# Performance work log

Measured on AMD Instinct MI355X. Metric: run time of the kernel, lower is better.

## Reference

```python
import jax, jax.numpy as jnp
import numpy as np

H = 256
G = H // 4
RBF = 16
CUTOFF = 10.0
N_ATOMS = 500000
N_BLOCKS = 50000


def _layernorm(x, g, b, eps=1e-5):
    m = jnp.mean(x, axis=-1, keepdims=True)
    v = jnp.var(x, axis=-1, keepdims=True)
    return (x - m) / jnp.sqrt(v + eps) * g + b


def setup_inputs() -> dict:
    key = jax.random.key(0)
    ks = jax.random.split(key, 16)
    def rn(k, shp, scale=0.02):
        return jax.random.normal(k, shp, dtype=jnp.float32) * scale
    return {
        "atom_features": jax.random.normal(ks[0], (N_ATOMS, H), dtype=jnp.float32),
        "atom_positions": jax.random.normal(ks[1], (N_ATOMS, 3), dtype=jnp.float32),
        "block_features": jax.random.normal(ks[2], (N_BLOCKS, H), dtype=jnp.float32),
        "block_id": jnp.sort(jax.random.randint(ks[3], (N_ATOMS,), 0, N_BLOCKS)),
        "rbf_centers": jnp.linspace(0.0, CUTOFF, RBF).astype(jnp.float32),
        "rbf_widths": jnp.full((RBF,), CUTOFF / RBF, dtype=jnp.float32),
        "Wg": rn(ks[4], (RBF, G)), "bg": jnp.zeros((G,), jnp.float32),
        "Wq": rn(ks[5], (H, H)), "bq": jnp.zeros((H,), jnp.float32),
        "Wk": rn(ks[6], (H + G, H)), "bk": jnp.zeros((H,), jnp.float32),
        "Wv": rn(ks[7], (H + G, H)), "bv": jnp.zeros((H,), jnp.float32),
        "Wc1": rn(ks[8], (H, H)), "bc1": jnp.zeros((H,), jnp.float32),
        "Wc2": rn(ks[9], (H, H)), "bc2": jnp.zeros((H,), jnp.float32),
        "Wf1": rn(ks[10], (H, 2 * H)), "bf1": jnp.zeros((2 * H,), jnp.float32),
        "Wf2": rn(ks[11], (2 * H, H)), "bf2": jnp.zeros((H,), jnp.float32),
        "ln1_g": jnp.ones((H,), jnp.float32), "ln1_b": jnp.zeros((H,), jnp.float32),
        "ln2_g": jnp.ones((H,), jnp.float32), "ln2_b": jnp.zeros((H,), jnp.float32),
    }


def reference(atom_features, atom_positions, block_features, block_id,
              rbf_centers, rbf_widths, Wg, bg, Wq, bq, Wk, bk, Wv, bv,
              Wc1, bc1, Wc2, bc2, Wf1, bf1, Wf2, bf2,
              ln1_g, ln1_b, ln2_g, ln2_b):
    nb = block_features.shape[0]
    seg = block_id
    # per-block geometry: centroid, relative distance, RBF expansion
    ones = jnp.ones((atom_features.shape[0],), atom_features.dtype)
    counts = jax.ops.segment_sum(ones, seg, num_segments=nb)
    centroids = jax.ops.segment_sum(atom_positions, seg, num_segments=nb) / jnp.maximum(counts, 1.0)[:, None]
    rel = atom_positions - centroids[seg]                      # [N, 3]
    d = jnp.linalg.norm(rel, axis=1)                           # [N]
    rbf = jnp.exp(-(d[:, None] - rbf_centers[None, :]) ** 2 / (2.0 * rbf_widths[None, :] ** 2))  # [N, RBF]
    geom = rbf @ Wg + bg                                       # [N, G]
    aug = jnp.concatenate([atom_features, geom], axis=1)       # [N, H+G]
    # cross-attention: one query per block, keys/values are block atoms
    Q = block_features @ Wq + bq                               # [NB, H]
    K = aug @ Wk + bk                                          # [N, H]
    V = aug @ Wv + bv                                          # [N, H]
    scale = 1.0 / np.sqrt(float(H))
    scores = jnp.sum(Q[seg] * K, axis=1) * scale               # [N]
    m = jax.ops.segment_max(scores, seg, num_segments=nb)
    m = jnp.where(jnp.isfinite(m), m, 0.0)
    e = jnp.exp(scores - m[seg])
    denom = jnp.maximum(jax.ops.segment_sum(e, seg, num_segments=nb), 1e-20)
    w = e / denom[seg]                                         # segment softmax weights
    context = jax.ops.segment_sum(w[:, None] * V, seg, num_segments=nb)  # [NB, H]
    upd = jax.nn.relu(context @ Wc1 + bc1) @ Wc2 + bc2         # context MLP (dropout=identity, eval)
    h = _layernorm(atom_features + upd[seg], ln1_g, ln1_b)     # scatter update back to atoms
    ffn = jax.nn.relu(h @ Wf1 + bf1) @ Wf2 + bf2
    return _layernorm(h + ffn, ln2_g, ln2_b)
```

## Files before the change

### kernel.cpp

```cpp
#include <hip/hip_runtime.h>
#include <hip/hip_bf16.h>


typedef __hip_bfloat16 bf16;
typedef __attribute__((ext_vector_type(8))) short bf16x8;
typedef __attribute__((ext_vector_type(4))) float f32x4;

__device__ __forceinline__ float b2f(bf16 v) { return __bfloat162float(v); }
__device__ __forceinline__ float us2f(unsigned short u) {
  union { unsigned int v; float f; } c; c.v = ((unsigned int)u) << 16; return c.f;
}
__device__ __forceinline__ unsigned short f2bu(float x) {
  bf16 t = __float2bfloat16(x);
  unsigned short u; __builtin_memcpy(&u, &t, 2); return u;
}
__device__ __forceinline__ float4 ld4(const float* p) {
  return *reinterpret_cast<const float4*>(p);
}
__device__ __forceinline__ float4 ldnt4(const float* p) {
  f32x4 v = __builtin_nontemporal_load(reinterpret_cast<const f32x4*>(p));
  return make_float4(v.x, v.y, v.z, v.w);
}
__device__ __forceinline__ float wsum(float v) {
#pragma unroll
  for (int o = 32; o > 0; o >>= 1) v += __shfl_xor(v, o, 64);
  return v;
}
__device__ __forceinline__ bf16x8 lds_frag(const unsigned short* base, int stride,
                                           int row, int k) {
  return *reinterpret_cast<const bf16x8*>(base + row * stride +
                                          (k ^ ((row & 7) << 3)));
}

__global__ void bounds_k(const int* __restrict__ seg, int* __restrict__ bs,
                         int* __restrict__ be, int N) {
  int i = blockIdx.x * 256 + threadIdx.x;
  if (i >= N) return;
  int b = seg[i];
  if (i == 0 || seg[i - 1] != b) bs[b] = i;
  if (i == N - 1 || seg[i + 1] != b) be[b] = i + 1;
}

__global__ void cent_k(const float* __restrict__ pos, const int* __restrict__ bs,
                       const int* __restrict__ be, float* __restrict__ cent, int NB) {
  int b = blockIdx.x * 256 + threadIdx.x;
  if (b >= NB) return;
  int s0 = bs[b], s1 = be[b];
  float sx = 0.f, sy = 0.f, sz = 0.f;
  for (int i = s0; i < s1; ++i) {
    sx += pos[(size_t)i * 3 + 0];
    sy += pos[(size_t)i * 3 + 1];
    sz += pos[(size_t)i * 3 + 2];
  }
  float inv = 1.f / fmaxf((float)(s1 - s0), 1.f);
  cent[(size_t)b * 3 + 0] = sx * inv;
  cent[(size_t)b * 3 + 1] = sy * inv;
  cent[(size_t)b * 3 + 2] = sz * inv;
}

__global__ __launch_bounds__(256) void geom_k(
    const float* __restrict__ pos, const int* __restrict__ seg,
    const float* __restrict__ cent, const float* __restrict__ centers,
    const float* __restrict__ widths, const float* __restrict__ Wg,
    const float* __restrict__ bg, bf16* __restrict__ geom, int N) {
  __shared__ float sWg[16][64];
  __shared__ float sc[16], sw[16], sbg[64];
  int t = threadIdx.x;
  if (t < 16) {
    sc[t] = centers[t];
    float w = widths[t];
    sw[t] = 1.f / (2.f * w * w);
  }
  for (int j = t; j < 1024; j += 256) sWg[j >> 6][j & 63] = Wg[j];
  if (t < 64) sbg[t] = bg[t];
  __syncthreads();
  int i = blockIdx.x * 256 + t;
  if (i >= N) return;
  int b = seg[i];
  float dx = pos[(size_t)i * 3 + 0] - cent[(size_t)b * 3 + 0];
  float dy = pos[(size_t)i * 3 + 1] - cent[(size_t)b * 3 + 1];
  float dz = pos[(size_t)i * 3 + 2] - cent[(size_t)b * 3 + 2];
  float d = sqrtf(dx * dx + dy * dy + dz * dz);
  float r[16];
#pragma unroll
  for (int j = 0; j < 16; ++j) {
    float dd = d - sc[j];
    r[j] = expf(-dd * dd * sw[j]);
  }
  bf16* gp = geom + (size_t)i * 64;
  for (int g0 = 0; g0 < 64; g0 += 4) {
    float a0 = sbg[g0], a1 = sbg[g0 + 1], a2 = sbg[g0 + 2], a3 = sbg[g0 + 3];
#pragma unroll
    for (int j = 0; j < 16; ++j) {
      float rj = r[j];
      a0 += rj * sWg[j][g0];
      a1 += rj * sWg[j][g0 + 1];
      a2 += rj * sWg[j][g0 + 2];
      a3 += rj * sWg[j][g0 + 3];
    }
    ushort4 o;
    o.x = f2bu(a0); o.y = f2bu(a1); o.z = f2bu(a2); o.w = f2bu(a3);
    *reinterpret_cast<ushort4*>(gp + g0) = o;
  }
}

__global__ void tr_k(const float* __restrict__ in, unsigned short* __restrict__ out,
                     int K, int N) {
  int idx = blockIdx.x * 256 + threadIdx.x;
  if (idx >= N * K) return;
  int n = idx / K, k = idx % K;
  out[idx] = f2bu(in[(size_t)k * N + n]);
}
__global__ void cast_k(const float* __restrict__ in, unsigned short* __restrict__ out,
                       int n) {
  int idx = blockIdx.x * 256 + threadIdx.x;
  if (idx < n) out[idx] = f2bu(in[idx]);
}

__global__ void pack1_k(const float* __restrict__ Wf1,
                        unsigned short* __restrict__ P) {
  int idx = blockIdx.x * 256 + threadIdx.x;
  if (idx >= 512 * 256) return;
  int e = idx & 7;
  int l = (idx >> 3) & 63;
  int blk = idx >> 9;
  int ks = blk & 7, wv = (blk >> 3) & 7, q = blk >> 6;
  int n = q * 128 + wv * 16 + (l & 15);
  int k = ks * 32 + (l >> 4) * 8 + e;
  P[idx] = f2bu(Wf1[(size_t)k * 512 + n]);
}
__global__ void pack2_k(const float* __restrict__ Wf2,
                        unsigned short* __restrict__ P) {
  int idx = blockIdx.x * 256 + threadIdx.x;
  if (idx >= 512 * 256) return;
  int e = idx & 7;
  int l = (idx >> 3) & 63;
  int blk = idx >> 9;
  int ks = blk & 3, q = (blk >> 2) & 3, nt = (blk >> 4) & 1, wv = blk >> 5;
  int n = wv * 32 + nt * 16 + (l & 15);
  int k = q * 128 + ks * 32 + (l >> 4) * 8 + e;
  P[idx] = f2bu(Wf2[(size_t)k * 256 + n]);
}

__global__ __launch_bounds__(512, 4) void blk1_k(
    const float* __restrict__ bfeat, const unsigned short* __restrict__ WqT,
    const float* __restrict__ bq, const unsigned short* __restrict__ WkC,
    const float* __restrict__ bk, float* __restrict__ u, float* __restrict__ cb,
    int NB) {
  __shared__ unsigned short x_lds[64 * 256];
  __shared__ unsigned short q_lds[64 * 256];
  const int t = threadIdx.x;
  const int lane = t & 63, wv = t >> 6, l15 = lane & 15, lhi = lane >> 4;
  const int r0 = blockIdx.x * 64;
  for (int rr = 0; rr < 8; ++rr) {
    int r = wv * 8 + rr;
    int row = r0 + r; if (row >= NB) row = NB - 1;
    float4 v = ldnt4(bfeat + (size_t)row * 256 + lane * 4);
    ushort4 o; o.x = f2bu(v.x); o.y = f2bu(v.y); o.z = f2bu(v.z); o.w = f2bu(v.w);
    *reinterpret_cast<ushort4*>(&x_lds[r * 256 + ((lane * 4) ^ ((r & 7) << 3))]) = o;
  }
  __syncthreads();
  {
    f32x4 acc[2][4];
#pragma unroll
    for (int nt = 0; nt < 2; ++nt)
#pragma unroll
      for (int rt = 0; rt < 4; ++rt) acc[nt][rt] = (f32x4){0.f, 0.f, 0.f, 0.f};
#pragma unroll
    for (int ks = 0; ks < 8; ++ks) {
      bf16x8 a[4];
#pragma unroll
      for (int rt = 0; rt < 4; ++rt)
        a[rt] = lds_frag(x_lds, 256, rt * 16 + l15, ks * 32 + lhi * 8);
#pragma unroll
      for (int nt = 0; nt < 2; ++nt) {
        bf16x8 b = *reinterpret_cast<const bf16x8*>(
            WqT + (size_t)(wv * 32 + nt * 16 + l15) * 256 + ks * 32 + lhi * 8);
#pragma unroll
        for (int rt = 0; rt < 4; ++rt)
          acc[nt][rt] = __builtin_amdgcn_mfma_f32_16x16x32_bf16(a[rt], b, acc[nt][rt], 0, 0, 0);
      }
    }
#pragma unroll
    for (int nt = 0; nt < 2; ++nt) {
      int col = wv * 32 + nt * 16 + l15;
      float bb = bq[col];
#pragma unroll
      for (int rt = 0; rt < 4; ++rt)
#pragma unroll
        for (int j = 0; j < 4; ++j) {
          int row = rt * 16 + lhi * 4 + j;
          q_lds[row * 256 + (col ^ ((row & 7) << 3))] = f2bu(acc[nt][rt][j] + bb);
        }
    }
  }
  __syncthreads();
  if (t < 64) {
    float a = 0.f;
    for (int c = 0; c < 256; ++c)
      a += us2f(q_lds[t * 256 + (c ^ ((t & 7) << 3))]) * bk[c];
    int row = r0 + t;
    if (row < NB) cb[row] = a;
  }
  for (int j = 0; j < 3; ++j) {
    int tile = wv + 8 * j;
    if (tile >= 20) break;
    f32x4 acc[4];
#pragma unroll
    for (int rt = 0; rt < 4; ++rt) acc[rt] = (f32x4){0.f, 0.f, 0.f, 0.f};
#pragma unroll
    for (int ks = 0; ks < 8; ++ks) {
      bf16x8 b = *reinterpret_cast<const bf16x8*>(
          WkC + (size_t)(tile * 16 + l15) * 256 + ks * 32 + lhi * 8);
#pragma unroll
      for (int rt = 0; rt < 4; ++rt) {
        bf16x8 a = lds_frag(q_lds, 256, rt * 16 + l15, ks * 32 + lhi * 8);
        acc[rt] = __builtin_amdgcn_mfma_f32_16x16x32_bf16(a, b, acc[rt], 0, 0, 0);
      }
    }
    int n = tile * 16 + l15;
#pragma unroll
    for (int rt = 0; rt < 4; ++rt)
#pragma unroll
      for (int jj = 0; jj < 4; ++jj) {
        int row = r0 + rt * 16 + lhi * 4 + jj;
        if (row < NB) u[(size_t)row * 320 + n] = acc[rt][jj];
      }
  }
}

__global__ __launch_bounds__(256) void attn_k(
    const float* __restrict__ feat, const bf16* __restrict__ geom,
    const float* __restrict__ u, const float* __restrict__ cbArr,
    const int* __restrict__ bs, const int* __restrict__ be,
    float* __restrict__ S, int NB) {
  int wave = threadIdx.x >> 6;
  int lane = threadIdx.x & 63;
  int b = blockIdx.x * 4 + wave;
  if (b >= NB) return;
  int s0 = bs[b], s1 = be[b];
  if (s1 <= s0) return;
  const float* ub = u + (size_t)b * 320;
  float4 uv = ld4(ub + lane * 4);
  float ug = ub[256 + lane];
  float cb = cbArr[b];
  const float scale = 0.0625f;
  float m = -1e30f, l = 0.f;
  float a0 = 0.f, a1 = 0.f, a2 = 0.f, a3 = 0.f, ag = 0.f;
  for (int i = s0; i < s1; ++i) {
    float4 f = ldnt4(feat + (size_t)i * 256 + lane * 4);
    float gm = b2f(geom[(size_t)i * 64 + lane]);
    float p = f.x * uv.x + f.y * uv.y + f.z * uv.z + f.w * uv.w + gm * ug;
    p = wsum(p);
    float s = (p + cb) * scale;
    if (s <= m) {
      float w = expf(s - m);
      l += w;
      a0 += w * f.x; a1 += w * f.y; a2 += w * f.z; a3 += w * f.w;
      ag += w * gm;
    } else {
      float corr = expf(m - s);
      l = l * corr + 1.f;
      a0 = a0 * corr + f.x; a1 = a1 * corr + f.y;
      a2 = a2 * corr + f.z; a3 = a3 * corr + f.w;
      ag = ag * corr + gm;
      m = s;
    }
  }
  float inv = 1.f / l;
  float* Sb = S + (size_t)b * 320;
  Sb[lane * 4 + 0] = a0 * inv; Sb[lane * 4 + 1] = a1 * inv;
  Sb[lane * 4 + 2] = a2 * inv; Sb[lane * 4 + 3] = a3 * inv;
  Sb[256 + lane] = ag * inv;
}

__global__ __launch_bounds__(512, 4) void blk2_k(
    const float* __restrict__ S, const unsigned short* __restrict__ WvT,
    const float* __restrict__ bv, const unsigned short* __restrict__ Wc1T,
    const float* __restrict__ bc1, const unsigned short* __restrict__ Wc2T,
    const float* __restrict__ bc2, float* __restrict__ upd, int NB) {
  __shared__ unsigned short s_lds[64 * 320];
  const int t = threadIdx.x;
  const int lane = t & 63, wv = t >> 6, l15 = lane & 15, lhi = lane >> 4;
  const int r0 = blockIdx.x * 64;
  for (int rr = 0; rr < 8; ++rr) {
    int r = wv * 8 + rr;
    int row = r0 + r; if (row >= NB) row = NB - 1;
    float4 v = ld4(S + (size_t)row * 320 + lane * 4);
    ushort4 o; o.x = f2bu(v.x); o.y = f2bu(v.y); o.z = f2bu(v.z); o.w = f2bu(v.w);
    *reinterpret_cast<ushort4*>(&s_lds[r * 320 + ((lane * 4) ^ ((r & 7) << 3))]) = o;
    float g = S[(size_t)row * 320 + 256 + lane];
    s_lds[r * 320 + ((256 + lane) ^ ((r & 7) << 3))] = f2bu(g);
  }
  __syncthreads();
  f32x4 acc[2][4];
#pragma unroll
  for (int nt = 0; nt < 2; ++nt)
#pragma unroll
    for (int rt = 0; rt < 4; ++rt) acc[nt][rt] = (f32x4){0.f, 0.f, 0.f, 0.f};
#pragma unroll
  for (int ks = 0; ks < 10; ++ks) {
    bf16x8 a[4];
#pragma unroll
    for (int rt = 0; rt < 4; ++rt)
      a[rt] = lds_frag(s_lds, 320, rt * 16 + l15, ks * 32 + lhi * 8);
#pragma unroll
    for (int nt = 0; nt < 2; ++nt) {
      bf16x8 b = *reinterpret_cast<const bf16x8*>(
          WvT + (size_t)(wv * 32 + nt * 16 + l15) * 320 + ks * 32 + lhi * 8);
#pragma unroll
      for (int rt = 0; rt < 4; ++rt)
        acc[nt][rt] = __builtin_amdgcn_mfma_f32_16x16x32_bf16(a[rt], b, acc[nt][rt], 0, 0, 0);
    }
  }
  __syncthreads();
#pragma unroll
  for (int nt = 0; nt < 2; ++nt) {
    int col = wv * 32 + nt * 16 + l15;
    float bb = bv[col];
#pragma unroll
    for (int rt = 0; rt < 4; ++rt)
#pragma unroll
      for (int j = 0; j < 4; ++j) {
        int row = rt * 16 + lhi * 4 + j;
        s_lds[row * 256 + (col ^ ((row & 7) << 3))] = f2bu(acc[nt][rt][j] + bb);
      }
  }
  __syncthreads();
#pragma unroll
  for (int nt = 0; nt < 2; ++nt)
#pragma unroll
    for (int rt = 0; rt < 4; ++rt) acc[nt][rt] = (f32x4){0.f, 0.f, 0.f, 0.f};
#pragma unroll
  for (int ks = 0; ks < 8; ++ks) {
    bf16x8 a[4];
#pragma unroll
    for (int rt = 0; rt < 4; ++rt)
      a[rt] = lds_frag(s_lds, 256, rt * 16 + l15, ks * 32 + lhi * 8);
#pragma unroll
    for (int nt = 0; nt < 2; ++nt) {
      bf16x8 b = *reinterpret_cast<const bf16x8*>(
          Wc1T + (size_t)(wv * 32 + nt * 16 + l15) * 256 + ks * 32 + lhi * 8);
#pragma unroll
      for (int rt = 0; rt < 4; ++rt)
        acc[nt][rt] = __builtin_amdgcn_mfma_f32_16x16x32_bf16(a[rt], b, acc[nt][rt], 0, 0, 0);
    }
  }
  __syncthreads();
#pragma unroll
  for (int nt = 0; nt < 2; ++nt) {
    int col = wv * 32 + nt * 16 + l15;
    float bb = bc1[col];
#pragma unroll
    for (int rt = 0; rt < 4; ++rt)
#pragma unroll
      for (int j = 0; j < 4; ++j) {
        int row = rt * 16 + lhi * 4 + j;
        s_lds[row * 256 + (col ^ ((row & 7) << 3))] = f2bu(fmaxf(acc[nt][rt][j] + bb, 0.f));
      }
  }
  __syncthreads();
#pragma unroll
  for (int nt = 0; nt < 2; ++nt)
#pragma unroll
    for (int rt = 0; rt < 4; ++rt) acc[nt][rt] = (f32x4){0.f, 0.f, 0.f, 0.f};
#pragma unroll
  for (int ks = 0; ks < 8; ++ks) {
    bf16x8 a[4];
#pragma unroll
    for (int rt = 0; rt < 4; ++rt)
      a[rt] = lds_frag(s_lds, 256, rt * 16 + l15, ks * 32 + lhi * 8);
#pragma unroll
    for (int nt = 0; nt < 2; ++nt) {
      bf16x8 b = *reinterpret_cast<const bf16x8*>(
          Wc2T + (size_t)(wv * 32 + nt * 16 + l15) * 256 + ks * 32 + lhi * 8);
#pragma unroll
      for (int rt = 0; rt < 4; ++rt)
        acc[nt][rt] = __builtin_amdgcn_mfma_f32_16x16x32_bf16(a[rt], b, acc[nt][rt], 0, 0, 0);
    }
  }
#pragma unroll
  for (int nt = 0; nt < 2; ++nt) {
    int col = wv * 32 + nt * 16 + l15;
    float bb = bc2[col];
#pragma unroll
    for (int rt = 0; rt < 4; ++rt)
#pragma unroll
      for (int j = 0; j < 4; ++j) {
        int row = r0 + rt * 16 + lhi * 4 + j;
        if (row < NB) upd[(size_t)row * 256 + col] = acc[nt][rt][j] + bb;
      }
  }
}

__global__ __launch_bounds__(512, 4) void ffn_mfma_k(
    const float* __restrict__ feat, const int* __restrict__ seg,
    const float* __restrict__ upd, const unsigned short* __restrict__ Wf1P,
    const float* __restrict__ bf1_, const unsigned short* __restrict__ Wf2P,
    const float* __restrict__ bf2_, const float* __restrict__ lng1,
    const float* __restrict__ lnb1, const float* __restrict__ lng2,
    const float* __restrict__ lnb2, float* __restrict__ out, int N) {
  __shared__ unsigned short h_lds[64 * 256];
  __shared__ unsigned short f1q_lds[64 * 136];
  const int t = threadIdx.x;
  const int lane = t & 63;
  const int wv = t >> 6;
  const int l15 = lane & 15;
  const int lhi = lane >> 4;
  const int r0 = blockIdx.x * 64;

  {
    float4 g1v = ld4(lng1 + lane * 4);
    float4 b1v = ld4(lnb1 + lane * 4);
    for (int rr = 0; rr < 8; ++rr) {
      int r = wv * 8 + rr;
      int row = r0 + r;
      if (row >= N) row = N - 1;
      int bidx = seg[row];
      float4 xf = ldnt4(feat + (size_t)row * 256 + lane * 4);
      float4 up = ld4(upd + (size_t)bidx * 256 + lane * 4);
      float x0 = xf.x + up.x, x1 = xf.y + up.y;
      float x2 = xf.z + up.z, x3 = xf.w + up.w;
      float s = wsum(x0 + x1 + x2 + x3);
      float s2 = wsum(x0 * x0 + x1 * x1 + x2 * x2 + x3 * x3);
      float mean = s * (1.f / 256.f);
      float var = s2 * (1.f / 256.f) - mean * mean;
      float rstd = rsqrtf(var + 1e-5f);
      ushort4 o;
      o.x = f2bu((x0 - mean) * rstd * g1v.x + b1v.x);
      o.y = f2bu((x1 - mean) * rstd * g1v.y + b1v.y);
      o.z = f2bu((x2 - mean) * rstd * g1v.z + b1v.z);
      o.w = f2bu((x3 - mean) * rstd * g1v.w + b1v.w);
      *reinterpret_cast<ushort4*>(&h_lds[r * 256 + ((lane * 4) ^ ((r & 7) << 3))]) = o;
    }
  }
  __syncthreads();

  f32x4 accC[2][4];
#pragma unroll
  for (int nt = 0; nt < 2; ++nt)
#pragma unroll
    for (int rt = 0; rt < 4; ++rt) accC[nt][rt] = (f32x4){0.f, 0.f, 0.f, 0.f};

#pragma unroll 1
  for (int q = 0; q < 4; ++q) {
    {
      f32x4 accB[4];
#pragma unroll
      for (int rt = 0; rt < 4; ++rt) accB[rt] = (f32x4){0.f, 0.f, 0.f, 0.f};
      const unsigned short* wb =
          Wf1P + (size_t)((q * 8 + wv) * 8) * 512 + lane * 8;
      bf16x8 bcur = *reinterpret_cast<const bf16x8*>(wb);
#pragma unroll
      for (int ks = 0; ks < 8; ++ks) {
        bf16x8 bnx = bcur;
        if (ks < 7) bnx = *reinterpret_cast<const bf16x8*>(wb + (ks + 1) * 512);
        int k = ks * 32 + lhi * 8;
        bf16x8 a0 = lds_frag(h_lds, 256, 0 * 16 + l15, k);
        bf16x8 a1 = lds_frag(h_lds, 256, 1 * 16 + l15, k);
        bf16x8 a2 = lds_frag(h_lds, 256, 2 * 16 + l15, k);
        bf16x8 a3 = lds_frag(h_lds, 256, 3 * 16 + l15, k);
        accB[0] = __builtin_amdgcn_mfma_f32_16x16x32_bf16(a0, bcur, accB[0], 0, 0, 0);
        accB[1] = __builtin_amdgcn_mfma_f32_16x16x32_bf16(a1, bcur, accB[1], 0, 0, 0);
        accB[2] = __builtin_amdgcn_mfma_f32_16x16x32_bf16(a2, bcur, accB[2], 0, 0, 0);
        accB[3] = __builtin_amdgcn_mfma_f32_16x16x32_bf16(a3, bcur, accB[3], 0, 0, 0);
        bcur = bnx;
      }
      int coll = wv * 16 + l15;
      float bb = bf1_[q * 128 + coll];
#pragma unroll
      for (int rt = 0; rt < 4; ++rt)
#pragma unroll
        for (int j = 0; j < 4; ++j) {
          int row = rt * 16 + lhi * 4 + j;
          f1q_lds[row * 136 + coll] = f2bu(fmaxf(accB[rt][j] + bb, 0.f));
        }
    }
    __syncthreads();
#pragma unroll
    for (int ks = 0; ks < 4; ++ks) {
      int k = ks * 32 + lhi * 8;
      bf16x8 a0 = *reinterpret_cast<const bf16x8*>(f1q_lds + (0 * 16 + l15) * 136 + k);
      bf16x8 a1 = *reinterpret_cast<const bf16x8*>(f1q_lds + (1 * 16 + l15) * 136 + k);
      bf16x8 a2 = *reinterpret_cast<const bf16x8*>(f1q_lds + (2 * 16 + l15) * 136 + k);
      bf16x8 a3 = *reinterpret_cast<const bf16x8*>(f1q_lds + (3 * 16 + l15) * 136 + k);
#pragma unroll
      for (int nt = 0; nt < 2; ++nt) {
        bf16x8 b = *reinterpret_cast<const bf16x8*>(
            Wf2P + (size_t)((wv * 2 + nt) * 16 + q * 4 + ks) * 512 + lane * 8);
        accC[nt][0] = __builtin_amdgcn_mfma_f32_16x16x32_bf16(a0, b, accC[nt][0], 0, 0, 0);
        accC[nt][1] = __builtin_amdgcn_mfma_f32_16x16x32_bf16(a1, b, accC[nt][1], 0, 0, 0);
        accC[nt][2] = __builtin_amdgcn_mfma_f32_16x16x32_bf16(a2, b, accC[nt][2], 0, 0, 0);
        accC[nt][3] = __builtin_amdgcn_mfma_f32_16x16x32_bf16(a3, b, accC[nt][3], 0, 0, 0);
      }
    }
    __syncthreads();
  }

#pragma unroll
  for (int nt = 0; nt < 2; ++nt) {
    int c = wv * 32 + nt * 16 + l15;
    float bb = bf2_[c];
#pragma unroll
    for (int rt = 0; rt < 4; ++rt)
#pragma unroll
      for (int j = 0; j < 4; ++j) {
        int row = rt * 16 + lhi * 4 + j;
        int idx = row * 256 + (c ^ ((row & 7) << 3));
        h_lds[idx] = f2bu(us2f(h_lds[idx]) + accC[nt][rt][j] + bb);
      }
  }
  __syncthreads();

  {
    float4 g2v = ld4(lng2 + lane * 4);
    float4 b2v = ld4(lnb2 + lane * 4);
    for (int rr = 0; rr < 8; ++rr) {
      int r = wv * 8 + rr;
      int row = r0 + r;
      if (row >= N) row = N - 1;
      int idx = r * 256 + ((lane * 4) ^ ((r & 7) << 3));
      ushort4 yv = *reinterpret_cast<const ushort4*>(&h_lds[idx]);
      float y0 = us2f(yv.x), y1 = us2f(yv.y), y2 = us2f(yv.z), y3 = us2f(yv.w);
      float s = wsum(y0 + y1 + y2 + y3);
      float s2 = wsum(y0 * y0 + y1 * y1 + y2 * y2 + y3 * y3);
      float mean = s * (1.f / 256.f);
      float var = s2 * (1.f / 256.f) - mean * mean;
      float rstd = rsqrtf(var + 1e-5f);
      float4 o;
      o.x = (y0 - mean) * rstd * g2v.x + b2v.x;
      o.y = (y1 - mean) * rstd * g2v.y + b2v.y;
      o.z = (y2 - mean) * rstd * g2v.z + b2v.z;
      o.w = (y3 - mean) * rstd * g2v.w + b2v.w;
      *reinterpret_cast<float4*>(out + (size_t)row * 256 + lane * 4) = o;
    }
  }
}

extern "C" void kernel_launch(void* const* d_in, const int* in_sizes, int n_in,
                              void* d_out, int out_size, void* d_ws, size_t ws_size,
                              hipStream_t stream) {
  const float* feat = (const float*)d_in[0];
  const float* pos = (const float*)d_in[1];
  const float* bfeat = (const float*)d_in[2];
  const int* seg = (const int*)d_in[3];
  const float* centers = (const float*)d_in[4];
  const float* widths = (const float*)d_in[5];
  const float* Wg = (const float*)d_in[6];
  const float* bg = (const float*)d_in[7];
  const float* Wq = (const float*)d_in[8];
  const float* bq = (const float*)d_in[9];
  const float* Wk = (const float*)d_in[10];
  const float* bk = (const float*)d_in[11];
  const float* Wv = (const float*)d_in[12];
  const float* bv = (const float*)d_in[13];
  const float* Wc1 = (const float*)d_in[14];
  const float* bc1 = (const float*)d_in[15];
  const float* Wc2 = (const float*)d_in[16];
  const float* bc2 = (const float*)d_in[17];
  const float* Wf1 = (const float*)d_in[18];
  const float* bf1_ = (const float*)d_in[19];
  const float* Wf2 = (const float*)d_in[20];
  const float* bf2_ = (const float*)d_in[21];
  const float* lng1 = (const float*)d_in[22];
  const float* lnb1 = (const float*)d_in[23];
  const float* lng2 = (const float*)d_in[24];
  const float* lnb2 = (const float*)d_in[25];
  float* out = (float*)d_out;

  const int N = in_sizes[0] / 256;
  const int NB = in_sizes[2] / 256;

  size_t off = 0;
  char* wsb = (char*)d_ws;
  auto alloc = [&](size_t bytes) -> void* {
    void* p = wsb + off;
    off += (bytes + 255) & ~(size_t)255;
    return p;
  };
  int* bs = (int*)alloc((size_t)NB * 4);
  int* be = (int*)alloc((size_t)NB * 4);
  float* cent = (float*)alloc((size_t)NB * 3 * 4);
  bf16* geom = (bf16*)alloc((size_t)N * 64 * 2);
  float* u = (float*)alloc((size_t)NB * 320 * 4);
  float* cb = (float*)alloc((size_t)NB * 4);
  float* S = (float*)alloc((size_t)NB * 320 * 4);
  float* upd = (float*)alloc((size_t)NB * 256 * 4);
  unsigned short* WqT = (unsigned short*)alloc((size_t)256 * 256 * 2);
  unsigned short* WkC = (unsigned short*)alloc((size_t)320 * 256 * 2);
  unsigned short* WvT = (unsigned short*)alloc((size_t)256 * 320 * 2);
  unsigned short* Wc1T = (unsigned short*)alloc((size_t)256 * 256 * 2);
  unsigned short* Wc2T = (unsigned short*)alloc((size_t)256 * 256 * 2);
  unsigned short* Wf1P = (unsigned short*)alloc((size_t)512 * 256 * 2);
  unsigned short* Wf2P = (unsigned short*)alloc((size_t)256 * 512 * 2);

  hipMemsetAsync(bs, 0, (size_t)NB * 4, stream);
  hipMemsetAsync(be, 0, (size_t)NB * 4, stream);

  tr_k<<<(256 * 256 + 255) / 256, 256, 0, stream>>>(Wq, WqT, 256, 256);
  cast_k<<<(320 * 256 + 255) / 256, 256, 0, stream>>>(Wk, WkC, 320 * 256);
  tr_k<<<(256 * 320 + 255) / 256, 256, 0, stream>>>(Wv, WvT, 320, 256);
  tr_k<<<(256 * 256 + 255) / 256, 256, 0, stream>>>(Wc1, Wc1T, 256, 256);
  tr_k<<<(256 * 256 + 255) / 256, 256, 0, stream>>>(Wc2, Wc2T, 256, 256);
  pack1_k<<<(512 * 256 + 255) / 256, 256, 0, stream>>>(Wf1, Wf1P);
  pack2_k<<<(512 * 256 + 255) / 256, 256, 0, stream>>>(Wf2, Wf2P);

  bounds_k<<<(N + 255) / 256, 256, 0, stream>>>(seg, bs, be, N);
  cent_k<<<(NB + 255) / 256, 256, 0, stream>>>(pos, bs, be, cent, NB);
  geom_k<<<(N + 255) / 256, 256, 0, stream>>>(pos, seg, cent, centers, widths,
                                              Wg, bg, geom, N);
  const int NBB = (NB + 63) / 64;
  blk1_k<<<NBB, 512, 0, stream>>>(bfeat, WqT, bq, WkC, bk, u, cb, NB);
  attn_k<<<(NB + 3) / 4, 256, 0, stream>>>(feat, geom, u, cb, bs, be, S, NB);
  blk2_k<<<NBB, 512, 0, stream>>>(S, WvT, bv, Wc1T, bc1, Wc2T, bc2, upd, NB);
  ffn_mfma_k<<<(N + 63) / 64, 512, 0, stream>>>(feat, seg, upd, Wf1P, bf1_, Wf2P,
                                                bf2_, lng1, lnb1, lng2, lnb2, out, N);
}
```

Measured before the change: 1.003 ms.

## Switch FFN kernel to 32x32x16 MFMA with 2x4 wave tiling

Replaces the 16x16x32 MFMA tiling in the fused FFN kernel with 32x32x16 MFMAs. Each wave now owns a 32-row by 32-column tile (waves split 2 by 4 over rows and columns) instead of all 64 rows by 16 columns. The Wf1/Wf2 packing kernels are reordered to match the new B-fragment layout. The f1 intermediate buffer drops its padding in favour of an XOR swizzle, and launch bounds rise to 6 blocks per CU to allow more occupancy, which may force register spills. The larger MFMA shape is meant to reduce LDS fragment reads per FLOP, though each wave now issues weight loads for every k-step without the previous prefetching.

```diff
diff --git a/kernel.cpp b/kernel.cpp
--- a/kernel.cpp
+++ b/kernel.cpp
@@ -5,6 +5,7 @@
 typedef __hip_bfloat16 bf16;
 typedef __attribute__((ext_vector_type(8))) short bf16x8;
 typedef __attribute__((ext_vector_type(4))) float f32x4;
+typedef __attribute__((ext_vector_type(16))) float f32x16;
 
 __device__ __forceinline__ float b2f(bf16 v) { return __bfloat162float(v); }
 __device__ __forceinline__ float us2f(unsigned short u) {
@@ -124,9 +125,9 @@
   int e = idx & 7;
   int l = (idx >> 3) & 63;
   int blk = idx >> 9;
-  int ks = blk & 7, wv = (blk >> 3) & 7, q = blk >> 6;
-  int n = q * 128 + wv * 16 + (l & 15);
-  int k = ks * 32 + (l >> 4) * 8 + e;
+  int kk = blk & 15, cb = (blk >> 4) & 3, q = blk >> 6;
+  int n = q * 128 + cb * 32 + (l & 31);
+  int k = kk * 16 + (l >> 5) * 8 + e;
   P[idx] = f2bu(Wf1[(size_t)k * 512 + n]);
 }
 __global__ void pack2_k(const float* __restrict__ Wf2,
@@ -136,9 +137,9 @@
   int e = idx & 7;
   int l = (idx >> 3) & 63;
   int blk = idx >> 9;
-  int ks = blk & 3, q = (blk >> 2) & 3, nt = (blk >> 4) & 1, wv = blk >> 5;
-  int n = wv * 32 + nt * 16 + (l & 15);
-  int k = q * 128 + ks * 32 + (l >> 4) * 8 + e;
+  int kk2 = blk & 7, q = (blk >> 3) & 3, cb = blk >> 5;
+  int n = cb * 32 + (l & 31);
+  int k = q * 128 + kk2 * 16 + (l >> 5) * 8 + e;
   P[idx] = f2bu(Wf2[(size_t)k * 256 + n]);
 }
 
@@ -393,7 +394,7 @@
   }
 }
 
-__global__ __launch_bounds__(512, 4) void ffn_mfma_k(
+__global__ __launch_bounds__(512, 6) void ffn_mfma_k(
     const float* __restrict__ feat, const int* __restrict__ seg,
     const float* __restrict__ upd, const unsigned short* __restrict__ Wf1P,
     const float* __restrict__ bf1_, const unsigned short* __restrict__ Wf2P,
@@ -401,12 +402,14 @@
     const float* __restrict__ lnb1, const float* __restrict__ lng2,
     const float* __restrict__ lnb2, float* __restrict__ out, int N) {
   __shared__ unsigned short h_lds[64 * 256];
-  __shared__ unsigned short f1q_lds[64 * 136];
+  __shared__ unsigned short f1q_lds[64 * 128];
   const int t = threadIdx.x;
   const int lane = t & 63;
   const int wv = t >> 6;
-  const int l15 = lane & 15;
-  const int lhi = lane >> 4;
+  const int rg = wv >> 2;
+  const int cg = wv & 3;
+  const int l31 = lane & 31;
+  const int kofs = (lane >> 5) * 8;
   const int r0 = blockIdx.x * 64;
 
   {
@@ -436,79 +439,68 @@
   }
   __syncthreads();
 
-  f32x4 accC[2][4];
-#pragma unroll
-  for (int nt = 0; nt < 2; ++nt)
-#pragma unroll
-    for (int rt = 0; rt < 4; ++rt) accC[nt][rt] = (f32x4){0.f, 0.f, 0.f, 0.f};
+  f32x16 accC0 = {};
+  f32x16 accC1 = {};
 
 #pragma unroll 1
   for (int q = 0; q < 4; ++q) {
+    f32x16 accB = {};
     {
-      f32x4 accB[4];
-#pragma unroll
-      for (int rt = 0; rt < 4; ++rt) accB[rt] = (f32x4){0.f, 0.f, 0.f, 0.f};
-      const unsigned short* wb =
-          Wf1P + (size_t)((q * 8 + wv) * 8) * 512 + lane * 8;
-      bf16x8 bcur = *reinterpret_cast<const bf16x8*>(wb);
-#pragma unroll
-      for (int ks = 0; ks < 8; ++ks) {
-        bf16x8 bnx = bcur;
-        if (ks < 7) bnx = *reinterpret_cast<const bf16x8*>(wb + (ks + 1) * 512);
-        int k = ks * 32 + lhi * 8;
-        bf16x8 a0 = lds_frag(h_lds, 256, 0 * 16 + l15, k);
-        bf16x8 a1 = lds_frag(h_lds, 256, 1 * 16 + l15, k);
-        bf16x8 a2 = lds_frag(h_lds, 256, 2 * 16 + l15, k);
-        bf16x8 a3 = lds_frag(h_lds, 256, 3 * 16 + l15, k);
-        accB[0] = __builtin_amdgcn_mfma_f32_16x16x32_bf16(a0, bcur, accB[0], 0, 0, 0);
-        accB[1] = __builtin_amdgcn_mfma_f32_16x16x32_bf16(a1, bcur, accB[1], 0, 0, 0);
-        accB[2] = __builtin_amdgcn_mfma_f32_16x16x32_bf16(a2, bcur, accB[2], 0, 0, 0);
-        accB[3] = __builtin_amdgcn_mfma_f32_16x16x32_bf16(a3, bcur, accB[3], 0, 0, 0);
-        bcur = bnx;
-      }
-      int coll = wv * 16 + l15;
-      float bb = bf1_[q * 128 + coll];
-#pragma unroll
-      for (int rt = 0; rt < 4; ++rt)
-#pragma unroll
-        for (int j = 0; j < 4; ++j) {
-          int row = rt * 16 + lhi * 4 + j;
-          f1q_lds[row * 136 + coll] = f2bu(fmaxf(accB[rt][j] + bb, 0.f));
-        }
+      const unsigned short* p1 = Wf1P + (size_t)((q * 4 + cg) * 16) * 512 + lane * 8;
+#pragma unroll
+      for (int kk = 0; kk < 16; ++kk) {
+        bf16x8 a = lds_frag(h_lds, 256, rg * 32 + l31, kk * 16 + kofs);
+        bf16x8 b = *reinterpret_cast<const bf16x8*>(p1 + kk * 512);
+        accB = __builtin_amdgcn_mfma_f32_32x32x16_bf16(a, b, accB, 0, 0, 0);
+      }
     }
     __syncthreads();
-#pragma unroll
-    for (int ks = 0; ks < 4; ++ks) {
-      int k = ks * 32 + lhi * 8;
-      bf16x8 a0 = *reinterpret_cast<const bf16x8*>(f1q_lds + (0 * 16 + l15) * 136 + k);
-      bf16x8 a1 = *reinterpret_cast<const bf16x8*>(f1q_lds + (1 * 16 + l15) * 136 + k);
-      bf16x8 a2 = *reinterpret_cast<const bf16x8*>(f1q_lds + (2 * 16 + l15) * 136 + k);
-      bf16x8 a3 = *reinterpret_cast<const bf16x8*>(f1q_lds + (3 * 16 + l15) * 136 + k);
-#pragma unroll
-      for (int nt = 0; nt < 2; ++nt) {
-        bf16x8 b = *reinterpret_cast<const bf16x8*>(
-            Wf2P + (size_t)((wv * 2 + nt) * 16 + q * 4 + ks) * 512 + lane * 8);
-        accC[nt][0] = __builtin_amdgcn_mfma_f32_16x16x32_bf16(a0, b, accC[nt][0], 0, 0, 0);
-        accC[nt][1] = __builtin_amdgcn_mfma_f32_16x16x32_bf16(a1, b, accC[nt][1], 0, 0, 0);
-        accC[nt][2] = __builtin_amdgcn_mfma_f32_16x16x32_bf16(a2, b, accC[nt][2], 0, 0, 0);
-        accC[nt][3] = __builtin_amdgcn_mfma_f32_16x16x32_bf16(a3, b, accC[nt][3], 0, 0, 0);
+    {
+      int col = cg * 32 + l31;
+      float bb = bf1_[q * 128 + col];
+#pragma unroll
+      for (int reg = 0; reg < 16; ++reg) {
+        int rl = (reg & 3) + 8 * (reg >> 2) + 4 * (lane >> 5);
+        int row = rg * 32 + rl;
+        f1q_lds[row * 128 + (col ^ ((row & 7) << 3))] =
+            f2bu(fmaxf(accB[reg] + bb, 0.f));
       }
     }
     __syncthreads();
-  }
-
-#pragma unroll
-  for (int nt = 0; nt < 2; ++nt) {
-    int c = wv * 32 + nt * 16 + l15;
-    float bb = bf2_[c];
-#pragma unroll
-    for (int rt = 0; rt < 4; ++rt)
-#pragma unroll
-      for (int j = 0; j < 4; ++j) {
-        int row = rt * 16 + lhi * 4 + j;
-        int idx = row * 256 + (c ^ ((row & 7) << 3));
-        h_lds[idx] = f2bu(us2f(h_lds[idx]) + accC[nt][rt][j] + bb);
-      }
+    {
+      const unsigned short* p2a = Wf2P + (size_t)((cg * 4 + q) * 8) * 512 + lane * 8;
+      const unsigned short* p2b = Wf2P + (size_t)(((cg + 4) * 4 + q) * 8) * 512 + lane * 8;
+#pragma unroll
+      for (int kk = 0; kk < 8; ++kk) {
+        bf16x8 a = lds_frag(f1q_lds, 128, rg * 32 + l31, kk * 16 + kofs);
+        bf16x8 b0 = *reinterpret_cast<const bf16x8*>(p2a + kk * 512);
+        bf16x8 b1 = *reinterpret_cast<const bf16x8*>(p2b + kk * 512);
+        accC0 = __builtin_amdgcn_mfma_f32_32x32x16_bf16(a, b0, accC0, 0, 0, 0);
+        accC1 = __builtin_amdgcn_mfma_f32_32x32x16_bf16(a, b1, accC1, 0, 0, 0);
+      }
+    }
+  }
+  __syncthreads();
+
+  {
+    int col0 = cg * 32 + l31;
+    float bb0 = bf2_[col0];
+#pragma unroll
+    for (int reg = 0; reg < 16; ++reg) {
+      int rl = (reg & 3) + 8 * (reg >> 2) + 4 * (lane >> 5);
+      int row = rg * 32 + rl;
+      int idx = row * 256 + (col0 ^ ((row & 7) << 3));
+      h_lds[idx] = f2bu(us2f(h_lds[idx]) + accC0[reg] + bb0);
+    }
+    int col1 = (cg + 4) * 32 + l31;
+    float bb1 = bf2_[col1];
+#pragma unroll
+    for (int reg = 0; reg < 16; ++reg) {
+      int rl = (reg & 3) + 8 * (reg >> 2) + 4 * (lane >> 5);
+      int row = rg * 32 + rl;
+      int idx = row * 256 + (col1 ^ ((row & 7) << 3));
+      h_lds[idx] = f2bu(us2f(h_lds[idx]) + accC1[reg] + bb1);
+    }
   }
   __syncthreads();
 
```

New measurement: 1.686 ms. 68.1% more time.
